# Performance work log

Measured on AMD Instinct MI355X. Metric: run time of the kernel, lower is better.

The kernel has to match this reference:

```python
import jax, jax.numpy as jnp
import numpy as np
import math

K = 10  # k_neighbors (k = min(10, N-1) = 10 since N=2048)


def setup_inputs() -> dict:
    key = jax.random.key(0)
    k1, k2, k3, k4 = jax.random.split(key, 4)
    N, T, H = 2048, 512, 256
    E_fixed = 65536
    x = jax.random.normal(k1, (N, T, H), dtype=jnp.float32)
    fixed_edge_index = jax.random.randint(k2, (2, E_fixed), 0, N, dtype=jnp.int64)
    fixed_edge_attr = jax.random.uniform(k3, (E_fixed, 1), dtype=jnp.float32)
    W = jax.random.normal(k4, (H // 2, H), dtype=jnp.float32) / math.sqrt(H)
    mix_alpha = 0.3
    mix_logit = jnp.array([math.log(mix_alpha / (1.0 - mix_alpha + 1e-08))], dtype=jnp.float32)
    return {"x": x, "fixed_edge_index": fixed_edge_index,
            "fixed_edge_attr": fixed_edge_attr, "W": W, "mix_logit": mix_logit}


def reference(x, fixed_edge_index, fixed_edge_attr, W, mix_logit):
    # x: [N, T, H]; W: [H//2, H]; mix_logit: [1]
    N = x.shape[0]
    x_agg = x.mean(axis=1)                                  # [N, H] temporal mean-pool
    e = x_agg @ W.T                                         # [N, H//2] bias-free projection
    e = e / jnp.maximum(jnp.linalg.norm(e, axis=-1, keepdims=True), 1e-12)  # F.normalize
    sim = e @ e.T                                           # [N, N] cosine similarity
    topk_vals, topk_idx = jax.lax.top_k(sim, K + 1)         # self-sim (=1) is in column 0
    topk_vals = topk_vals[:, 1:]                            # [N, K] drop self-loop
    topk_idx = topk_idx[:, 1:]
    src = jnp.repeat(jnp.arange(N, dtype=fixed_edge_index.dtype), K)  # [N*K]
    dst = topk_idx.reshape(-1).astype(fixed_edge_index.dtype)
    dyn_edge_index = jnp.stack([src, dst], axis=0)          # [2, N*K]
    dyn_edge_attr = topk_vals.reshape(-1, 1)                # [N*K, 1]
    alpha = jax.nn.sigmoid(mix_logit[0])
    combined_edge_index = jnp.concatenate([fixed_edge_index, dyn_edge_index], axis=1)
    combined_edge_attr = jnp.concatenate(
        [fixed_edge_attr * (1.0 - alpha), dyn_edge_attr * alpha], axis=0)
    return combined_edge_index, combined_edge_attr
```

## Files before the change

kernel.cpp:

```cpp
#include <hip/hip_runtime.h>
#include <hip/hip_bf16.h>
#include <math.h>

typedef float f4 __attribute__((ext_vector_type(4)));


__global__ __launch_bounds__(1024) void mean_kernel(const float* __restrict__ x,
                                                    float* __restrict__ xagg,
                                                    int T, int H, int N) {
    const int tid = threadIdx.x;
    const int v   = tid & 63;
    const int tg  = tid >> 6;

    __shared__ f4 red[1024];

    for (int n = blockIdx.x; n < N; n += gridDim.x) {
        const f4* xr = reinterpret_cast<const f4*>(x + (size_t)n * T * H);
        f4 a0 = {0.f, 0.f, 0.f, 0.f}, a1 = a0, a2 = a0, a3 = a0;
        for (int m = 0; m < 32; m += 4) {
            f4 d0 = xr[(tg + 16 * (m + 0)) * 64 + v];
            f4 d1 = xr[(tg + 16 * (m + 1)) * 64 + v];
            f4 d2 = xr[(tg + 16 * (m + 2)) * 64 + v];
            f4 d3 = xr[(tg + 16 * (m + 3)) * 64 + v];
            a0 += d0; a1 += d1; a2 += d2; a3 += d3;
        }
        red[tid] = (a0 + a1) + (a2 + a3);
        __syncthreads();
        if (tid < 64) {
            f4 o = {0.f, 0.f, 0.f, 0.f};
            #pragma unroll
            for (int w = 0; w < 16; ++w) o += red[tid + w * 64];
            o *= (1.0f / (float)T);
            reinterpret_cast<f4*>(xagg + (size_t)n * H)[v] = o;
        }
        __syncthreads();
    }
}

__global__ __launch_bounds__(128) void proj_norm_kernel(const float* __restrict__ xagg,
                                                        const float* __restrict__ W,
                                                        float* __restrict__ e,
                                                        int H ) {
    const int n = blockIdx.x;
    const int j = threadIdx.x;

    __shared__ float xs[256];
    xs[j]       = xagg[(size_t)n * H + j];
    xs[j + 128] = xagg[(size_t)n * H + j + 128];
    __syncthreads();

    const float* Wr = W + (size_t)j * H;
    float acc = 0.f;
    #pragma unroll 8
    for (int c = 0; c < 256; ++c) acc = fmaf(Wr[c], xs[c], acc);

    float s = acc * acc;
    #pragma unroll
    for (int off = 32; off; off >>= 1) s += __shfl_xor(s, off);
    __shared__ float nrm[2];
    if ((j & 63) == 0) nrm[j >> 6] = s;
    __syncthreads();
    float tot = nrm[0] + nrm[1];
    float inv = 1.0f / fmaxf(sqrtf(tot), 1e-12f);
    e[(size_t)n * 128 + j] = acc * inv;
}

#define TK_ROWS 4
__global__ __launch_bounds__(256) void simtopk_kernel(const float* __restrict__ e,
                                                      const float* __restrict__ mix,
                                                      float* __restrict__ out,
                                                      int N , int E ) {
    __shared__ float eL[TK_ROWS][128];
    __shared__ float simL[TK_ROWS][2048];

    const int i0  = blockIdx.x * TK_ROWS;
    const int tid = threadIdx.x;
    const int M   = E + N * 10;

    {
        int r = tid >> 6;
        int c = tid & 63;
        const float* er = e + (size_t)(i0 + r) * 128;
        eL[r][c]      = er[c];
        eL[r][c + 64] = er[c + 64];
    }
    __syncthreads();

    for (int j = tid; j < N; j += 256) {
        const f4* ej = reinterpret_cast<const f4*>(e + (size_t)j * 128);
        float acc[TK_ROWS] = {0.f, 0.f, 0.f, 0.f};
        #pragma unroll 4
        for (int c4 = 0; c4 < 32; ++c4) {
            f4 vv = ej[c4];
            #pragma unroll
            for (int r = 0; r < TK_ROWS; ++r) {
                const float* el = &eL[r][c4 * 4];
                acc[r] = fmaf(vv.x, el[0], acc[r]);
                acc[r] = fmaf(vv.y, el[1], acc[r]);
                acc[r] = fmaf(vv.z, el[2], acc[r]);
                acc[r] = fmaf(vv.w, el[3], acc[r]);
            }
        }
        #pragma unroll
        for (int r = 0; r < TK_ROWS; ++r) simL[r][j] = acc[r];
    }
    __syncthreads();

    const int w    = tid >> 6;
    const int lane = tid & 63;
    const int i    = i0 + w;
    const float alpha = 1.0f / (1.0f + expf(-mix[0]));

    float keepv = 0.f;
    int   keepi = 0;
    for (int round = 0; round < 11; ++round) {
        float bv = -3.0f;
        int   bi = N;
        for (int t = 0; t < 32; ++t) {
            int j = t * 64 + lane;
            float v = simL[w][j];
            if (v > bv || (v == bv && j < bi)) { bv = v; bi = j; }
        }
        #pragma unroll
        for (int off = 32; off; off >>= 1) {
            float ov = __shfl_xor(bv, off);
            int   oi = __shfl_xor(bi, off);
            if (ov > bv || (ov == bv && oi < bi)) { bv = ov; bi = oi; }
        }
        if ((bi & 63) == lane && bi < N) simL[w][bi] = -3.0f;
        if (lane == round) { keepv = bv; keepi = bi; }
    }
    if (lane >= 1 && lane <= 10) {
        int kk  = lane - 1;
        int pos = i * 10 + kk;
        out[(size_t)E + pos]         = (float)i;
        out[(size_t)M + E + pos]     = (float)keepi;
        out[2 * (size_t)M + E + pos] = keepv * alpha;
    }
}

__global__ __launch_bounds__(256) void fixed_kernel(const int* __restrict__ ei,
                                                    const float* __restrict__ ea,
                                                    const float* __restrict__ mix,
                                                    float* __restrict__ out,
                                                    int E, int M) {
    const int idx = blockIdx.x * blockDim.x + threadIdx.x;
    if (idx < E) {
        float alpha = 1.0f / (1.0f + expf(-mix[0]));
        out[idx]                 = (float)ei[idx];
        out[(size_t)M + idx]     = (float)ei[E + idx];
        out[2 * (size_t)M + idx] = ea[idx] * (1.0f - alpha);
    }
}

extern "C" void kernel_launch(void* const* d_in, const int* in_sizes, int n_in,
                              void* d_out, int out_size, void* d_ws, size_t ws_size,
                              hipStream_t stream) {
    const float* x   = (const float*)d_in[0];
    const int*   ei  = (const int*)d_in[1];
    const float* ea  = (const float*)d_in[2];
    const float* W   = (const float*)d_in[3];
    const float* mix = (const float*)d_in[4];

    const int H  = 256;
    const int E  = in_sizes[2];
    const int M  = out_size / 3;
    const int N  = (M - E) / 10;
    const int T  = (int)((size_t)in_sizes[0] / ((size_t)N * H));

    float* xagg = (float*)d_ws;
    float* e    = xagg + (size_t)N * H;
    float* out  = (float*)d_out;

    mean_kernel<<<512, 1024, 0, stream>>>(x, xagg, T, H, N);
    proj_norm_kernel<<<N, 128, 0, stream>>>(xagg, W, e, H);
    simtopk_kernel<<<N / TK_ROWS, 256, 0, stream>>>(e, mix, out, N, E);
    fixed_kernel<<<(E + 255) / 256, 256, 0, stream>>>(ei, ea, mix, out, E, M);
}
```

Measured before the change: 336.8 us.

## Split temporal mean into two-stage chunked reduction across many small blocks

Replaces the persistent 512-block mean kernel with a first stage that launches one 256-thread block per 64-timestep chunk (8 chunks per node) and writes partial sums to workspace. A second small kernel combines the 8 partials per node and scales by 1/T. The aim is more blocks in flight and more loads outstanding when streaming the 2 GB input, which should raise achieved HBM bandwidth. The cost is an extra launch and a partial-sum round trip. It also hardcodes T=512 and H=256 in the chunking and assumes the workspace has room for the partial buffer.

```diff
diff --git a/kernel.cpp b/kernel.cpp
--- a/kernel.cpp
+++ b/kernel.cpp
@@ -5,36 +5,42 @@
 typedef float f4 __attribute__((ext_vector_type(4)));
 
 
-__global__ __launch_bounds__(1024) void mean_kernel(const float* __restrict__ x,
-                                                    float* __restrict__ xagg,
-                                                    int T, int H, int N) {
-    const int tid = threadIdx.x;
-    const int v   = tid & 63;
-    const int tg  = tid >> 6;
+__global__ __launch_bounds__(256) void mean_stageA(const float* __restrict__ x,
+                                                   float* __restrict__ part) {
+    const int bid  = blockIdx.x;
+    const int tid  = threadIdx.x;
+    const int lane = tid & 63;
 
-    __shared__ f4 red[1024];
+    const f4* xc = reinterpret_cast<const f4*>(x) + (size_t)bid * 4096;
+    f4 a0 = {0.f, 0.f, 0.f, 0.f}, a1 = a0, a2 = a0, a3 = a0;
+    #pragma unroll
+    for (int k = 0; k < 16; k += 4) {
+        f4 d0 = xc[(k + 0) * 256 + tid];
+        f4 d1 = xc[(k + 1) * 256 + tid];
+        f4 d2 = xc[(k + 2) * 256 + tid];
+        f4 d3 = xc[(k + 3) * 256 + tid];
+        a0 += d0; a1 += d1; a2 += d2; a3 += d3;
+    }
+    __shared__ f4 red[256];
+    red[tid] = (a0 + a1) + (a2 + a3);
+    __syncthreads();
+    if (tid < 64) {
+        f4 o = (red[lane] + red[lane + 64]) + (red[lane + 128] + red[lane + 192]);
+        reinterpret_cast<f4*>(part)[(size_t)bid * 64 + lane] = o;
+    }
+}
 
-    for (int n = blockIdx.x; n < N; n += gridDim.x) {
-        const f4* xr = reinterpret_cast<const f4*>(x + (size_t)n * T * H);
-        f4 a0 = {0.f, 0.f, 0.f, 0.f}, a1 = a0, a2 = a0, a3 = a0;
-        for (int m = 0; m < 32; m += 4) {
-            f4 d0 = xr[(tg + 16 * (m + 0)) * 64 + v];
-            f4 d1 = xr[(tg + 16 * (m + 1)) * 64 + v];
-            f4 d2 = xr[(tg + 16 * (m + 2)) * 64 + v];
-            f4 d3 = xr[(tg + 16 * (m + 3)) * 64 + v];
-            a0 += d0; a1 += d1; a2 += d2; a3 += d3;
-        }
-        red[tid] = (a0 + a1) + (a2 + a3);
-        __syncthreads();
-        if (tid < 64) {
-            f4 o = {0.f, 0.f, 0.f, 0.f};
-            #pragma unroll
-            for (int w = 0; w < 16; ++w) o += red[tid + w * 64];
-            o *= (1.0f / (float)T);
-            reinterpret_cast<f4*>(xagg + (size_t)n * H)[v] = o;
-        }
-        __syncthreads();
-    }
+__global__ __launch_bounds__(64) void mean_stageB(const float* __restrict__ part,
+                                                  float* __restrict__ xagg,
+                                                  int T) {
+    const int n = blockIdx.x;
+    const int j = threadIdx.x;
+    const f4* p = reinterpret_cast<const f4*>(part) + (size_t)n * 8 * 64;
+    f4 o = {0.f, 0.f, 0.f, 0.f};
+    #pragma unroll
+    for (int c = 0; c < 8; ++c) o += p[c * 64 + j];
+    o *= (1.0f / (float)T);
+    reinterpret_cast<f4*>(xagg)[(size_t)n * 64 + j] = o;
 }
 
 __global__ __launch_bounds__(128) void proj_norm_kernel(const float* __restrict__ xagg,
@@ -170,9 +176,12 @@
 
     float* xagg = (float*)d_ws;
     float* e    = xagg + (size_t)N * H;
+    float* part = e + (size_t)N * 128;
     float* out  = (float*)d_out;
 
-    mean_kernel<<<512, 1024, 0, stream>>>(x, xagg, T, H, N);
+    const int nchunks = N * 8;
+    mean_stageA<<<nchunks, 256, 0, stream>>>(x, part);
+    mean_stageB<<<N, 64, 0, stream>>>(part, xagg, T);
     proj_norm_kernel<<<N, 128, 0, stream>>>(xagg, W, e, H);
     simtopk_kernel<<<N / TK_ROWS, 256, 0, stream>>>(e, mix, out, N, E);
     fixed_kernel<<<(E + 255) / 256, 256, 0, stream>>>(ei, ea, mix, out, E, M);
```

After: 322.0 us. -4.4%, faster.
